# Kernel optimization log

Hardware: AMD Instinct MI355X
Metric: run time of the kernel (lower is better)

Reference implementation:

```python
import jax, jax.numpy as jnp
import numpy as np

EPS = 1e-12


def setup_inputs() -> dict:
    key = jax.random.key(0)
    k1, k2, k3 = jax.random.split(key, 3)
    N, D, K = 262144, 64, 1024
    input_data = jax.random.normal(k1, (N, D), dtype=jnp.float32)
    random_vector = jax.random.normal(k2, (N, D), dtype=jnp.float32)
    # HeUniform over (K, D): limit = sqrt(6 / fan_in) with fan_in = K
    limit = np.sqrt(6.0 / K)
    codebooks = jax.random.uniform(k3, (K, D), dtype=jnp.float32, minval=-limit, maxval=limit)
    codebooks_used = jnp.zeros((K,), dtype=jnp.int32)
    return {"input_data": input_data, "random_vector": random_vector,
            "codebooks": codebooks, "codebooks_used": codebooks_used}


def reference(input_data, random_vector, codebooks, codebooks_used):
    # training=True path of NSVQ.call
    K = codebooks.shape[0]
    N = input_data.shape[0]
    sim = input_data @ codebooks.T
    dists = (jnp.sum(input_data * input_data, axis=1, keepdims=True)
             + jnp.sum(codebooks * codebooks, axis=1)[None, :]
             - 2.0 * sim)
    min_indices = jnp.argmin(dists, axis=1)                      # [N]
    hard_q = codebooks[min_indices]                              # [N, D]
    # NSVQ noise substitution
    res_norm = jnp.sqrt(jnp.sum((input_data - hard_q) ** 2, axis=1, keepdims=True))
    rv_norm = jnp.sqrt(jnp.sum(random_vector ** 2, axis=1, keepdims=True))
    vq_error = (res_norm / (rv_norm + EPS)) * random_vector
    quantized_input = input_data + vq_error
    # perplexity from code usage histogram
    counts = jax.ops.segment_sum(jnp.ones((N,), dtype=jnp.float32), min_indices,
                                 num_segments=K)                 # [K]
    avg_probs = counts / jnp.float32(N)
    perplexity = jnp.exp(-jnp.sum(avg_probs * jnp.log(avg_probs + EPS)))
    codebooks_used_new = codebooks_used + counts.astype(jnp.int32)
    return quantized_input, perplexity, codebooks_used_new
```

## Files before the change

### kernel.cpp

```cpp
#include <hip/hip_runtime.h>
#include <math.h>


#define NROWS 262144
#define DIM 64
#define KCODES 1024
#define ND ((size_t)NROWS * DIM)

typedef __attribute__((ext_vector_type(8))) short bf16x8;
typedef __attribute__((ext_vector_type(4))) float f32x4;

__device__ inline short f2bf(float f) {
    unsigned u = __builtin_bit_cast(unsigned, f);
    unsigned r = (u + 0x7FFFu + ((u >> 16) & 1u)) >> 16;
    return (short)r;
}
__device__ inline float bf2f(short h) {
    unsigned u = ((unsigned)(unsigned short)h) << 16;
    return __builtin_bit_cast(float, u);
}

typedef const __attribute__((address_space(1))) void* as1p;
typedef __attribute__((address_space(3))) void* as3p;
__device__ inline void gl_lds16(const void* g, void* l) {
    __builtin_amdgcn_global_load_lds((as1p)g, (as3p)l, 16, 0, 0);
}

__global__ __launch_bounds__(256) void nsvq_prep(
    const float* __restrict__ cb, short* __restrict__ cbs,
    float* __restrict__ cnorm)
{
    const int tid = blockIdx.x * 256 + threadIdx.x;
    const int k = tid >> 3;
    const int u = tid & 7;
    const float* p = cb + (size_t)k * DIM + u * 8;
    float4 f0 = *(const float4*)p;
    float4 f1 = *(const float4*)(p + 4);
    float fv[8] = {f0.x, f0.y, f0.z, f0.w, f1.x, f1.y, f1.z, f1.w};

    float s = 0.f;
    bf16x8 hv, lv;
#pragma unroll
    for (int j = 0; j < 8; ++j) {
        s = fmaf(fv[j], fv[j], s);
        float f = -2.0f * fv[j];
        short hi = f2bf(f);
        hv[j] = hi;
        lv[j] = f2bf(f - bf2f(hi));
    }
#pragma unroll
    for (int o = 1; o < 8; o <<= 1) s += __shfl_xor(s, o, 64);

    const size_t base = (size_t)(k >> 7) * 16384 + (size_t)u * 1024 + (size_t)(k & 127) * 8;
    *(bf16x8*)(cbs + base) = hv;
    *(bf16x8*)(cbs + base + 8192) = lv;
    if (u == 0) cnorm[k] = s;
}

__global__ __launch_bounds__(256) void nsvq_mfma(
    const float* __restrict__ x, const short* __restrict__ cbs,
    const float* __restrict__ cnorm, int* __restrict__ bestk_out)
{
    __shared__ short lds[16384];

    const int tid  = threadIdx.x;
    const int lane = tid & 63;
    const int wave = tid >> 6;
    const int q    = lane >> 4;
    const int n    = lane & 15;
    const int wBase = blockIdx.x * 256 + wave * 64;

    bf16x8 ah[4][2], al[4][2];
#pragma unroll
    for (int s = 0; s < 4; ++s) {
        const int row = wBase + s * 16 + n;
#pragma unroll
        for (int c2 = 0; c2 < 2; ++c2) {
            const float* p = x + (size_t)row * DIM + c2 * 32 + q * 8;
            float4 g0 = *(const float4*)p;
            float4 g1 = *(const float4*)(p + 4);
            float fv[8] = {g0.x, g0.y, g0.z, g0.w, g1.x, g1.y, g1.z, g1.w};
#pragma unroll
            for (int j = 0; j < 8; ++j) {
                short hi = f2bf(fv[j]);
                ah[s][c2][j] = hi;
                al[s][c2][j] = f2bf(fv[j] - bf2f(hi));
            }
        }
    }

    float best[4][4];
    int   bidx[4][4];
#pragma unroll
    for (int s = 0; s < 4; ++s)
#pragma unroll
        for (int r = 0; r < 4; ++r) { best[s][r] = 3.4e38f; bidx[s][r] = 0; }

    for (int chunk = 0; chunk < 8; ++chunk) {
        const short* src = cbs + (size_t)chunk * 16384;
#pragma unroll
        for (int r = 0; r < 8; ++r) {
            const int idx = r * 256 + tid;
            gl_lds16(src + idx * 8, lds + idx * 8);
        }
        float cn[8];
#pragma unroll
        for (int t = 0; t < 8; ++t) cn[t] = cnorm[chunk * 128 + t * 16 + n];

        __syncthreads();

#pragma unroll
        for (int t = 0; t < 8; ++t) {
            const int ci = (t * 16 + n) * 8;
            bf16x8 bh0 = *(const bf16x8*)(lds + q * 1024 + ci);
            bf16x8 bh1 = *(const bf16x8*)(lds + (q + 4) * 1024 + ci);
            bf16x8 bl0 = *(const bf16x8*)(lds + 8192 + q * 1024 + ci);
            bf16x8 bl1 = *(const bf16x8*)(lds + 8192 + (q + 4) * 1024 + ci);
            f32x4 cnv = {cn[t], cn[t], cn[t], cn[t]};
            const int code = chunk * 128 + t * 16 + n;

#pragma unroll
            for (int s = 0; s < 4; ++s) {
                f32x4 a = cnv;
                a = __builtin_amdgcn_mfma_f32_16x16x32_bf16(ah[s][0], bh0, a, 0, 0, 0);
                a = __builtin_amdgcn_mfma_f32_16x16x32_bf16(ah[s][1], bh1, a, 0, 0, 0);
                a = __builtin_amdgcn_mfma_f32_16x16x32_bf16(al[s][0], bh0, a, 0, 0, 0);
                a = __builtin_amdgcn_mfma_f32_16x16x32_bf16(al[s][1], bh1, a, 0, 0, 0);
                a = __builtin_amdgcn_mfma_f32_16x16x32_bf16(ah[s][0], bl0, a, 0, 0, 0);
                a = __builtin_amdgcn_mfma_f32_16x16x32_bf16(ah[s][1], bl1, a, 0, 0, 0);
#pragma unroll
                for (int r = 0; r < 4; ++r) {
                    if (a[r] < best[s][r]) { best[s][r] = a[r]; bidx[s][r] = code; }
                }
            }
        }
        __syncthreads();
    }

#pragma unroll
    for (int o = 1; o < 16; o <<= 1) {
#pragma unroll
        for (int s = 0; s < 4; ++s)
#pragma unroll
            for (int r = 0; r < 4; ++r) {
                float od = __shfl_xor(best[s][r], o, 64);
                int   ok = __shfl_xor(bidx[s][r], o, 64);
                if (od < best[s][r] || (od == best[s][r] && ok < bidx[s][r])) {
                    best[s][r] = od; bidx[s][r] = ok;
                }
            }
    }
    if (n == 0) {
#pragma unroll
        for (int s = 0; s < 4; ++s)
#pragma unroll
            for (int r = 0; r < 4; ++r)
                bestk_out[wBase + s * 16 + q * 4 + r] = bidx[s][r];
    }
}

__global__ __launch_bounds__(256) void nsvq_epilogue(
    const float* __restrict__ x, const float* __restrict__ rv,
    const float* __restrict__ cb, const int* __restrict__ bestk_in,
    float* __restrict__ out, unsigned int* __restrict__ counts)
{
    const int lane = threadIdx.x & 63;
    const int wave = threadIdx.x >> 6;
    const int sub = lane >> 4;
    const int c16 = lane & 15;
    const int row = (blockIdx.x * 4 + wave) * 4 + sub;
    const size_t off = (size_t)row * DIM + c16 * 4;

    float4 xv  = *(const float4*)(x + off);
    float4 rvv = *(const float4*)(rv + off);
    const int bk = bestk_in[row];
    float4 cv = *(const float4*)(cb + (size_t)bk * DIM + c16 * 4);

    float d0 = xv.x - cv.x, d1 = xv.y - cv.y, d2 = xv.z - cv.z, d3 = xv.w - cv.w;
    float res = fmaf(d0, d0, fmaf(d1, d1, fmaf(d2, d2, d3 * d3)));
    float rr  = fmaf(rvv.x, rvv.x, fmaf(rvv.y, rvv.y, fmaf(rvv.z, rvv.z, rvv.w * rvv.w)));
#pragma unroll
    for (int o = 1; o < 16; o <<= 1) {
        res += __shfl_xor(res, o, 64);
        rr  += __shfl_xor(rr, o, 64);
    }
    float scale = sqrtf(res) / (sqrtf(rr) + 1e-12f);

    float4 ov;
    ov.x = fmaf(scale, rvv.x, xv.x);
    ov.y = fmaf(scale, rvv.y, xv.y);
    ov.z = fmaf(scale, rvv.z, xv.z);
    ov.w = fmaf(scale, rvv.w, xv.w);
    *(float4*)(out + off) = ov;

    if (c16 == 0) atomicAdd(&counts[bk], 1u);
}

__global__ void nsvq_finalize(const unsigned int* __restrict__ counts,
                              const int* __restrict__ used,
                              float* __restrict__ out)
{
    const int k = threadIdx.x;
    const unsigned c = counts[k];
    float avg = (float)c * (1.0f / (float)NROWS);
    float term = (c > 0) ? (-avg * logf(avg + 1e-12f)) : 0.0f;

    float v = term;
#pragma unroll
    for (int o = 32; o > 0; o >>= 1) v += __shfl_down(v, o, 64);

    __shared__ float partial[16];
    if ((threadIdx.x & 63) == 0) partial[threadIdx.x >> 6] = v;
    __syncthreads();

    if (threadIdx.x < 64) {
        float s = (threadIdx.x < 16) ? partial[threadIdx.x] : 0.0f;
#pragma unroll
        for (int o = 32; o > 0; o >>= 1) s += __shfl_down(s, o, 64);
        if (threadIdx.x == 0) out[ND] = expf(s);
    }
    out[ND + 1 + k] = (float)(c + (unsigned)used[k]);
}

extern "C" void kernel_launch(void* const* d_in, const int* in_sizes, int n_in,
                              void* d_out, int out_size, void* d_ws, size_t ws_size,
                              hipStream_t stream) {
    const float* x    = (const float*)d_in[0];
    const float* rv   = (const float*)d_in[1];
    const float* cb   = (const float*)d_in[2];
    const int*   used = (const int*)d_in[3];
    float* out = (float*)d_out;

    char* ws = (char*)d_ws;
    unsigned int* counts = (unsigned int*)ws;
    float*        cnorm  = (float*)(ws + 4096);
    short*        cbs    = (short*)(ws + 8192);
    int*          bestk  = (int*)(ws + 8192 + 262144);

    hipMemsetAsync(counts, 0, KCODES * sizeof(unsigned int), stream);
    nsvq_prep<<<KCODES * 8 / 256, 256, 0, stream>>>(cb, cbs, cnorm);
    nsvq_mfma<<<NROWS / 256, 256, 0, stream>>>(x, cbs, cnorm, bestk);
    nsvq_epilogue<<<NROWS / 16, 256, 0, stream>>>(x, rv, cb, bestk, out, counts);
    nsvq_finalize<<<1, KCODES, 0, stream>>>(counts, used, out);
}
```

Before: 314.1 us.

## Fuse nearest-code search and noise-substitution epilogue into one kernel

Merges the MFMA argmin kernel and the epilogue kernel into one. The residual norm is now computed algebraically as ||x||^2 plus the best distance, so the codebook row is no longer gathered, x is kept in registers instead of re-read, and the bestk round-trip through global memory is gone. Rows per block drop from 256 to 128 to make room for the extra registers, which doubles how often each block reloads the codebook into LDS. The residual norm now carries the bf16-split dot-product error, and a clamp at zero guards against cancellation.

```diff
diff --git a/kernel.cpp b/kernel.cpp
--- a/kernel.cpp
+++ b/kernel.cpp
@@ -57,9 +57,10 @@
     if (u == 0) cnorm[k] = s;
 }
 
-__global__ __launch_bounds__(256) void nsvq_mfma(
-    const float* __restrict__ x, const short* __restrict__ cbs,
-    const float* __restrict__ cnorm, int* __restrict__ bestk_out)
+__global__ __launch_bounds__(256) void nsvq_fused(
+    const float* __restrict__ x, const float* __restrict__ rv,
+    const short* __restrict__ cbs, const float* __restrict__ cnorm,
+    float* __restrict__ out, unsigned int* __restrict__ counts)
 {
     __shared__ short lds[16384];
 
@@ -68,31 +69,42 @@
     const int wave = tid >> 6;
     const int q    = lane >> 4;
     const int n    = lane & 15;
-    const int wBase = blockIdx.x * 256 + wave * 64;
-
-    bf16x8 ah[4][2], al[4][2];
-#pragma unroll
-    for (int s = 0; s < 4; ++s) {
+    const int wBase = blockIdx.x * 128 + wave * 32;
+
+    float  xf[2][16];
+    bf16x8 ah[2][2], al[2][2];
+    float  xx[2];
+#pragma unroll
+    for (int s = 0; s < 2; ++s) {
         const int row = wBase + s * 16 + n;
+        float acc = 0.f;
 #pragma unroll
         for (int c2 = 0; c2 < 2; ++c2) {
             const float* p = x + (size_t)row * DIM + c2 * 32 + q * 8;
             float4 g0 = *(const float4*)p;
             float4 g1 = *(const float4*)(p + 4);
-            float fv[8] = {g0.x, g0.y, g0.z, g0.w, g1.x, g1.y, g1.z, g1.w};
+            xf[s][c2 * 8 + 0] = g0.x; xf[s][c2 * 8 + 1] = g0.y;
+            xf[s][c2 * 8 + 2] = g0.z; xf[s][c2 * 8 + 3] = g0.w;
+            xf[s][c2 * 8 + 4] = g1.x; xf[s][c2 * 8 + 5] = g1.y;
+            xf[s][c2 * 8 + 6] = g1.z; xf[s][c2 * 8 + 7] = g1.w;
 #pragma unroll
             for (int j = 0; j < 8; ++j) {
-                short hi = f2bf(fv[j]);
+                float f = xf[s][c2 * 8 + j];
+                acc = fmaf(f, f, acc);
+                short hi = f2bf(f);
                 ah[s][c2][j] = hi;
-                al[s][c2][j] = f2bf(fv[j] - bf2f(hi));
-            }
-        }
-    }
-
-    float best[4][4];
-    int   bidx[4][4];
-#pragma unroll
-    for (int s = 0; s < 4; ++s)
+                al[s][c2][j] = f2bf(f - bf2f(hi));
+            }
+        }
+        acc += __shfl_xor(acc, 16, 64);
+        acc += __shfl_xor(acc, 32, 64);
+        xx[s] = acc;
+    }
+
+    float best[2][4];
+    int   bidx[2][4];
+#pragma unroll
+    for (int s = 0; s < 2; ++s)
 #pragma unroll
         for (int r = 0; r < 4; ++r) { best[s][r] = 3.4e38f; bidx[s][r] = 0; }
 
@@ -120,7 +132,7 @@
             const int code = chunk * 128 + t * 16 + n;
 
 #pragma unroll
-            for (int s = 0; s < 4; ++s) {
+            for (int s = 0; s < 2; ++s) {
                 f32x4 a = cnv;
                 a = __builtin_amdgcn_mfma_f32_16x16x32_bf16(ah[s][0], bh0, a, 0, 0, 0);
                 a = __builtin_amdgcn_mfma_f32_16x16x32_bf16(ah[s][1], bh1, a, 0, 0, 0);
@@ -140,7 +152,7 @@
 #pragma unroll
     for (int o = 1; o < 16; o <<= 1) {
 #pragma unroll
-        for (int s = 0; s < 4; ++s)
+        for (int s = 0; s < 2; ++s)
 #pragma unroll
             for (int r = 0; r < 4; ++r) {
                 float od = __shfl_xor(best[s][r], o, 64);
@@ -150,50 +162,64 @@
                 }
             }
     }
+
+    float* resf = (float*)lds;
     if (n == 0) {
 #pragma unroll
-        for (int s = 0; s < 4; ++s)
-#pragma unroll
-            for (int r = 0; r < 4; ++r)
-                bestk_out[wBase + s * 16 + q * 4 + r] = bidx[s][r];
-    }
-}
-
-__global__ __launch_bounds__(256) void nsvq_epilogue(
-    const float* __restrict__ x, const float* __restrict__ rv,
-    const float* __restrict__ cb, const int* __restrict__ bestk_in,
-    float* __restrict__ out, unsigned int* __restrict__ counts)
-{
-    const int lane = threadIdx.x & 63;
-    const int wave = threadIdx.x >> 6;
-    const int sub = lane >> 4;
-    const int c16 = lane & 15;
-    const int row = (blockIdx.x * 4 + wave) * 4 + sub;
-    const size_t off = (size_t)row * DIM + c16 * 4;
-
-    float4 xv  = *(const float4*)(x + off);
-    float4 rvv = *(const float4*)(rv + off);
-    const int bk = bestk_in[row];
-    float4 cv = *(const float4*)(cb + (size_t)bk * DIM + c16 * 4);
-
-    float d0 = xv.x - cv.x, d1 = xv.y - cv.y, d2 = xv.z - cv.z, d3 = xv.w - cv.w;
-    float res = fmaf(d0, d0, fmaf(d1, d1, fmaf(d2, d2, d3 * d3)));
-    float rr  = fmaf(rvv.x, rvv.x, fmaf(rvv.y, rvv.y, fmaf(rvv.z, rvv.z, rvv.w * rvv.w)));
-#pragma unroll
-    for (int o = 1; o < 16; o <<= 1) {
-        res += __shfl_xor(res, o, 64);
-        rr  += __shfl_xor(rr, o, 64);
-    }
-    float scale = sqrtf(res) / (sqrtf(rr) + 1e-12f);
-
-    float4 ov;
-    ov.x = fmaf(scale, rvv.x, xv.x);
-    ov.y = fmaf(scale, rvv.y, xv.y);
-    ov.z = fmaf(scale, rvv.z, xv.z);
-    ov.w = fmaf(scale, rvv.w, xv.w);
-    *(float4*)(out + off) = ov;
-
-    if (c16 == 0) atomicAdd(&counts[bk], 1u);
+        for (int s = 0; s < 2; ++s)
+#pragma unroll
+            for (int r = 0; r < 4; ++r) {
+                const int rl = wave * 32 + s * 16 + q * 4 + r;
+                resf[rl] = best[s][r];
+                atomicAdd(&counts[bidx[s][r]], 1u);
+            }
+    }
+    __syncthreads();
+
+#pragma unroll
+    for (int s = 0; s < 2; ++s) {
+        const int row = wBase + s * 16 + n;
+        float res2 = xx[s] + resf[wave * 32 + s * 16 + n];
+        if (res2 < 0.f) res2 = 0.f;
+        float resn = sqrtf(res2);
+
+        float rvf[16];
+        float rr = 0.f;
+#pragma unroll
+        for (int c2 = 0; c2 < 2; ++c2) {
+            const float* p = rv + (size_t)row * DIM + c2 * 32 + q * 8;
+            float4 g0 = *(const float4*)p;
+            float4 g1 = *(const float4*)(p + 4);
+            rvf[c2 * 8 + 0] = g0.x; rvf[c2 * 8 + 1] = g0.y;
+            rvf[c2 * 8 + 2] = g0.z; rvf[c2 * 8 + 3] = g0.w;
+            rvf[c2 * 8 + 4] = g1.x; rvf[c2 * 8 + 5] = g1.y;
+            rvf[c2 * 8 + 6] = g1.z; rvf[c2 * 8 + 7] = g1.w;
+#pragma unroll
+            for (int j = 0; j < 8; ++j) {
+                float f = rvf[c2 * 8 + j];
+                rr = fmaf(f, f, rr);
+            }
+        }
+        rr += __shfl_xor(rr, 16, 64);
+        rr += __shfl_xor(rr, 32, 64);
+        float scale = resn / (sqrtf(rr) + 1e-12f);
+
+#pragma unroll
+        for (int c2 = 0; c2 < 2; ++c2) {
+            float4 o0, o1;
+            o0.x = fmaf(scale, rvf[c2 * 8 + 0], xf[s][c2 * 8 + 0]);
+            o0.y = fmaf(scale, rvf[c2 * 8 + 1], xf[s][c2 * 8 + 1]);
+            o0.z = fmaf(scale, rvf[c2 * 8 + 2], xf[s][c2 * 8 + 2]);
+            o0.w = fmaf(scale, rvf[c2 * 8 + 3], xf[s][c2 * 8 + 3]);
+            o1.x = fmaf(scale, rvf[c2 * 8 + 4], xf[s][c2 * 8 + 4]);
+            o1.y = fmaf(scale, rvf[c2 * 8 + 5], xf[s][c2 * 8 + 5]);
+            o1.z = fmaf(scale, rvf[c2 * 8 + 6], xf[s][c2 * 8 + 6]);
+            o1.w = fmaf(scale, rvf[c2 * 8 + 7], xf[s][c2 * 8 + 7]);
+            float* op = out + (size_t)row * DIM + c2 * 32 + q * 8;
+            *(float4*)op = o0;
+            *(float4*)(op + 4) = o1;
+        }
+    }
 }
 
 __global__ void nsvq_finalize(const unsigned int* __restrict__ counts,
@@ -235,11 +261,9 @@
     unsigned int* counts = (unsigned int*)ws;
     float*        cnorm  = (float*)(ws + 4096);
     short*        cbs    = (short*)(ws + 8192);
-    int*          bestk  = (int*)(ws + 8192 + 262144);
 
     hipMemsetAsync(counts, 0, KCODES * sizeof(unsigned int), stream);
     nsvq_prep<<<KCODES * 8 / 256, 256, 0, stream>>>(cb, cbs, cnorm);
-    nsvq_mfma<<<NROWS / 256, 256, 0, stream>>>(x, cbs, cnorm, bestk);
-    nsvq_epilogue<<<NROWS / 16, 256, 0, stream>>>(x, rv, cb, bestk, out, counts);
+    nsvq_fused<<<NROWS / 128, 256, 0, stream>>>(x, rv, cbs, cnorm, out, counts);
     nsvq_finalize<<<1, KCODES, 0, stream>>>(counts, used, out);
 }
```

After: 270.0 us. 14.0% less time.
